# Kernel optimization log

Measured on AMD Instinct MI355X. Metric: run time of the kernel, lower is better.

Reference implementation:

```python
import jax, jax.numpy as jnp
import numpy as np

N = 100000   # nodes
E = 1600000  # edges
D = 128      # input feat
H = 128      # hidden
C = 2        # out classes
EPS = 1e-5


def setup_inputs() -> dict:
    key = jax.random.key(0)
    ks = jax.random.split(key, 12)
    s = 0.05
    return {
        "x": jax.random.normal(ks[0], (N, D), jnp.float32),
        "W1": jax.random.normal(ks[1], (D, H), jnp.float32) * s,
        "b1": jnp.zeros((H,), jnp.float32),
        "g1": jnp.ones((H,), jnp.float32),
        "be1": jnp.zeros((H,), jnp.float32),
        "W2": jax.random.normal(ks[2], (H, H), jnp.float32) * s,
        "b2": jnp.zeros((H,), jnp.float32),
        "g2": jnp.ones((H,), jnp.float32),
        "be2": jnp.zeros((H,), jnp.float32),
        "W3": jax.random.normal(ks[3], (H, C), jnp.float32) * s,
        "b3": jnp.zeros((C,), jnp.float32),
        "edge_index": jax.random.randint(ks[4], (2, E), 0, N, dtype=jnp.int32),
    }


def _gcn_conv(x, W, b, src, dst, dis, di):
    h = x @ W                                   # [N, H]
    coef = (dis[src] * dis[dst])[:, None]       # per-edge norm
    msg = h[src] * coef                         # [E, H] gather
    agg = jax.ops.segment_sum(msg, dst, num_segments=x.shape[0])  # scatter-add
    agg = agg + h * di[:, None]                 # self-loop term (1/deg_i)
    return agg + b


def _bn(x, g, be):
    mu = x.mean(0)
    var = x.var(0)
    return (x - mu) * jax.lax.rsqrt(var + EPS) * g + be


def reference(x, W1, b1, g1, be1, W2, b2, g2, be2, W3, b3, edge_index):
    src, dst = edge_index[0], edge_index[1]
    n = x.shape[0]
    deg = jax.ops.segment_sum(jnp.ones((src.shape[0],), x.dtype), dst, num_segments=n) + 1.0
    dis = jax.lax.rsqrt(deg)
    di = 1.0 / deg
    h = jax.nn.relu(_bn(_gcn_conv(x, W1, b1, src, dst, dis, di), g1, be1))
    h = jax.nn.relu(_bn(_gcn_conv(h, W2, b2, src, dst, dis, di), g2, be2))
    h = _gcn_conv(h, W3, b3, src, dst, dis, di)
    return jax.nn.softmax(h, axis=1)
```

## Files before the change

kernel.cpp:

```cpp
#include <hip/hip_runtime.h>

#define NN 100000
#define NE 1600000
#define DF 128
#define NH (NN * DF)
#define EPS 1e-5f
#define NB 196
#define CAP 10240
#define EPB 8192
#define STB 512

typedef unsigned int uint;
typedef unsigned short ushort;
typedef __attribute__((ext_vector_type(8))) short bf16x8;
typedef __attribute__((ext_vector_type(4))) float f32x4;

__device__ __forceinline__ ushort f2bf(float f) {
    uint u = __float_as_uint(f);
    u += 0x7fffu + ((u >> 16) & 1u);
    return (ushort)(u >> 16);
}
__device__ __forceinline__ float bflo(uint u) { return __uint_as_float(u << 16); }
__device__ __forceinline__ float bfhi(uint u) { return __uint_as_float(u & 0xffff0000u); }

__launch_bounds__(256)
__global__ void k_part(const int* __restrict__ src, const int* __restrict__ dst,
                       int* __restrict__ gcur, uint* __restrict__ ebuf) {
    __shared__ int cnt[NB], base[NB];
    int t = threadIdx.x;
    if (t < NB) cnt[t] = 0;
    __syncthreads();
    int e0 = blockIdx.x * EPB;
#pragma unroll
    for (int i = 0; i < EPB / 256; ++i) {
        int e = e0 + i * 256 + t;
        if (e < NE) atomicAdd(&cnt[dst[e] >> 9], 1);
    }
    __syncthreads();
    if (t < NB) {
        base[t] = atomicAdd(&gcur[t], cnt[t]);
        cnt[t] = 0;
    }
    __syncthreads();
#pragma unroll
    for (int i = 0; i < EPB / 256; ++i) {
        int e = e0 + i * 256 + t;
        if (e < NE) {
            int d = dst[e];
            int b = d >> 9;
            int off = atomicAdd(&cnt[b], 1);
            ebuf[b * CAP + base[b] + off] = (uint)src[e] | ((uint)(d & 511) << 17);
        }
    }
}

__global__ void k_bscan(const int* __restrict__ gcur, int* __restrict__ bstart,
                        int* __restrict__ rp) {
    __shared__ int sh[256];
    int t = threadIdx.x;
    int v = (t < NB) ? gcur[t] : 0;
    sh[t] = v;
    __syncthreads();
    for (int off = 1; off < 256; off <<= 1) {
        int x = (t >= off) ? sh[t - off] : 0;
        __syncthreads();
        sh[t] += x;
        __syncthreads();
    }
    if (t < NB) bstart[t] = sh[t] - v;
    if (t == 0) {
        bstart[NB] = NE;
        rp[NN] = NE;
    }
}

__launch_bounds__(256)
__global__ void k_c1(const uint* __restrict__ ebuf, const int* __restrict__ gcur,
                     const int* __restrict__ bstart, float* __restrict__ dis,
                     float* __restrict__ di, int* __restrict__ rp) {
    __shared__ int ncnt[512];
    __shared__ int ssum[256];
    int b = blockIdx.x, t = threadIdx.x;
    ncnt[t] = 0;
    ncnt[t + 256] = 0;
    __syncthreads();
    int ne = gcur[b];
    const uint* eb = ebuf + (size_t)b * CAP;
    for (int e = t; e < ne; e += 256) atomicAdd(&ncnt[eb[e] >> 17], 1);
    __syncthreads();
    int a0 = ncnt[t * 2], a1 = ncnt[t * 2 + 1];
    int ps = a0 + a1;
    ssum[t] = ps;
    __syncthreads();
    for (int off = 1; off < 256; off <<= 1) {
        int x = (t >= off) ? ssum[t - off] : 0;
        __syncthreads();
        ssum[t] += x;
        __syncthreads();
    }
    int excl = ssum[t] - ps;
    int base = bstart[b];
    int g0 = b * 512 + t * 2;
    if (g0 < NN) {
        rp[g0] = base + excl;
        float d = (float)a0 + 1.0f;
        dis[g0] = rsqrtf(d);
        di[g0] = 1.0f / d;
    }
    if (g0 + 1 < NN) {
        rp[g0 + 1] = base + excl + a0;
        float d = (float)a1 + 1.0f;
        dis[g0 + 1] = rsqrtf(d);
        di[g0 + 1] = 1.0f / d;
    }
}

__launch_bounds__(256)
__global__ void k_c2(const uint* __restrict__ ebuf, const int* __restrict__ gcur,
                     const int* __restrict__ rp, const float* __restrict__ dis,
                     uint2* __restrict__ ec) {
    __shared__ int cur[512];
    __shared__ float dl[512];
    int b = blockIdx.x, t = threadIdx.x;
#pragma unroll
    for (int i = 0; i < 2; ++i) {
        int g = b * 512 + t + i * 256;
        if (g < NN) {
            cur[t + i * 256] = rp[g];
            dl[t + i * 256] = dis[g];
        }
    }
    __syncthreads();
    int ne = gcur[b];
    const uint* eb = ebuf + (size_t)b * CAP;
    for (int e = t; e < ne; e += 256) {
        uint u = eb[e];
        int s = u & 0x1FFFF;
        int dloc = u >> 17;
        int pos = atomicAdd(&cur[dloc], 1);
        ec[pos] = make_uint2((uint)s, __float_as_uint(dis[s] * dl[dloc]));
    }
}

__global__ void k_cvt_x(const float* __restrict__ X, ushort* __restrict__ Xb) {
    int t = blockIdx.x * blockDim.x + threadIdx.x;
    if (t >= NH / 8) return;
    const float4* X4 = (const float4*)X;
    float4 v0 = X4[t * 2], v1 = X4[t * 2 + 1];
    uint4 o;
    o.x = (uint)f2bf(v0.x) | ((uint)f2bf(v0.y) << 16);
    o.y = (uint)f2bf(v0.z) | ((uint)f2bf(v0.w) << 16);
    o.z = (uint)f2bf(v1.x) | ((uint)f2bf(v1.y) << 16);
    o.w = (uint)f2bf(v1.z) | ((uint)f2bf(v1.w) << 16);
    ((uint4*)Xb)[t] = o;
}

__global__ void k_cvt_w(const float* __restrict__ W, ushort* __restrict__ Wt) {
    int id = blockIdx.x * blockDim.x + threadIdx.x;
    int n = id & 127, k = id >> 7;
    ushort b = f2bf(W[id]);
    int byte = n * 256 + (((k >> 3) ^ (n & 7)) << 4) + ((k & 7) << 1);
    *(ushort*)((char*)Wt + byte) = b;
}

__launch_bounds__(256, 2)
__global__ void k_mm_mfma(const ushort* __restrict__ Xb, const ushort* __restrict__ Wt,
                          const float* __restrict__ par, ushort* __restrict__ Y,
                          int nrows) {
    __shared__ uint4 ws4[2048];
    char* ws = (char*)ws4;
    const int tid = threadIdx.x;
    const int wv = tid >> 6, l = tid & 63;
    const int l15 = l & 15, l4 = l >> 4;
    const int row_base = blockIdx.x * 128 + wv * 32;
    const bool act = row_base < nrows;

    bf16x8 a[2][4];
    if (act) {
#pragma unroll
        for (int mt = 0; mt < 2; ++mt)
#pragma unroll
            for (int ks = 0; ks < 4; ++ks) {
                int r = row_base + mt * 16 + l15;
                a[mt][ks] = *(const bf16x8*)&Xb[(size_t)r * 128 + ks * 32 + l4 * 8];
            }
        if (par) {
#pragma unroll
            for (int ks = 0; ks < 4; ++ks) {
                int k0 = ks * 32 + l4 * 8;
                float4 sa = *(const float4*)&par[k0];
                float4 sb = *(const float4*)&par[k0 + 4];
                float4 ha = *(const float4*)&par[128 + k0];
                float4 hb = *(const float4*)&par[128 + k0 + 4];
                float sc[8] = {sa.x, sa.y, sa.z, sa.w, sb.x, sb.y, sb.z, sb.w};
                float sh[8] = {ha.x, ha.y, ha.z, ha.w, hb.x, hb.y, hb.z, hb.w};
#pragma unroll
                for (int mt = 0; mt < 2; ++mt)
#pragma unroll
                    for (int j = 0; j < 8; ++j) {
                        float f = __uint_as_float(((uint)(ushort)a[mt][ks][j]) << 16);
                        f = fmaxf(f * sc[j] + sh[j], 0.0f);
                        a[mt][ks][j] = (short)f2bf(f);
                    }
            }
        }
    }
    const uint4* Wg = (const uint4*)Wt;
#pragma unroll
    for (int i = 0; i < 8; ++i) ws4[tid + i * 256] = Wg[tid + i * 256];
    __syncthreads();
    if (!act) return;

    f32x4 acc[2][8];
#pragma unroll
    for (int mt = 0; mt < 2; ++mt)
#pragma unroll
        for (int nt = 0; nt < 8; ++nt) acc[mt][nt] = (f32x4){0.f, 0.f, 0.f, 0.f};

#pragma unroll
    for (int ks = 0; ks < 4; ++ks) {
        bf16x8 b[8];
#pragma unroll
        for (int nt = 0; nt < 8; ++nt) {
            int n = nt * 16 + l15;
            int chunk = (ks * 4 + l4) ^ (n & 7);
            b[nt] = *(const bf16x8*)(ws + n * 256 + chunk * 16);
        }
#pragma unroll
        for (int nt = 0; nt < 8; ++nt) {
            acc[0][nt] = __builtin_amdgcn_mfma_f32_16x16x32_bf16(a[0][ks], b[nt], acc[0][nt], 0, 0, 0);
            acc[1][nt] = __builtin_amdgcn_mfma_f32_16x16x32_bf16(a[1][ks], b[nt], acc[1][nt], 0, 0, 0);
        }
    }
#pragma unroll
    for (int mt = 0; mt < 2; ++mt)
#pragma unroll
        for (int nt = 0; nt < 8; ++nt)
#pragma unroll
            for (int r = 0; r < 4; ++r) {
                int ro = row_base + mt * 16 + l4 * 4 + r;
                Y[(size_t)ro * 128 + nt * 16 + l15] = f2bf(acc[mt][nt][r]);
            }
}

__launch_bounds__(256)
__global__ void k_gather_b(const ushort* __restrict__ H, const int* __restrict__ rp,
                           const uint2* __restrict__ ec, const float* __restrict__ di,
                           const float* __restrict__ b, uint* __restrict__ outb) {
    int wid = (int)(((long long)blockIdx.x * blockDim.x + threadIdx.x) >> 6);
    int lane = threadIdx.x & 63;
    if (wid >= NN) return;
    int beg = rp[wid], end = rp[wid + 1];
    float dv = di[wid];
    const uint* H32 = (const uint*)H;
    uint hu = H32[(size_t)wid * 64 + lane];
    float2 bb = *(const float2*)&b[lane * 2];
    float ax = bflo(hu) * dv + bb.x;
    float ay = bfhi(hu) * dv + bb.y;
    int i = beg;
    for (; i + 3 < end; i += 4) {
        uint2 e0 = ec[i], e1 = ec[i + 1], e2 = ec[i + 2], e3 = ec[i + 3];
        uint u0 = H32[(size_t)e0.x * 64 + lane];
        uint u1 = H32[(size_t)e1.x * 64 + lane];
        uint u2 = H32[(size_t)e2.x * 64 + lane];
        uint u3 = H32[(size_t)e3.x * 64 + lane];
        float c0 = __uint_as_float(e0.y), c1 = __uint_as_float(e1.y);
        float c2 = __uint_as_float(e2.y), c3 = __uint_as_float(e3.y);
        ax += bflo(u0) * c0 + bflo(u1) * c1 + bflo(u2) * c2 + bflo(u3) * c3;
        ay += bfhi(u0) * c0 + bfhi(u1) * c1 + bfhi(u2) * c2 + bfhi(u3) * c3;
    }
    for (; i < end; ++i) {
        uint2 e0 = ec[i];
        uint u = H32[(size_t)e0.x * 64 + lane];
        float c = __uint_as_float(e0.y);
        ax += bflo(u) * c;
        ay += bfhi(u) * c;
    }
    outb[(size_t)wid * 64 + lane] = (uint)f2bf(ax) | ((uint)f2bf(ay) << 16);
}

__launch_bounds__(256)
__global__ void k_statsb(const uint* __restrict__ V, float* __restrict__ partial,
                         int nrows) {
    int cp = threadIdx.x & 63;
    int q = threadIdx.x >> 6;
    float s0 = 0.f, s1 = 0.f, q0 = 0.f, q1 = 0.f;
    for (int r = blockIdx.x * 4 + q; r < nrows; r += STB * 4) {
        uint u = V[(size_t)r * 64 + cp];
        float lo = bflo(u), hi = bfhi(u);
        s0 += lo;
        q0 += lo * lo;
        s1 += hi;
        q1 += hi * hi;
    }
    __shared__ float L[4][256];
    L[0][threadIdx.x] = s0;
    L[1][threadIdx.x] = s1;
    L[2][threadIdx.x] = q0;
    L[3][threadIdx.x] = q1;
    __syncthreads();
    if (q == 0) {
        float a = 0.f, b = 0.f, c = 0.f, d = 0.f;
#pragma unroll
        for (int j = 0; j < 4; ++j) {
            a += L[0][cp + j * 64];
            b += L[1][cp + j * 64];
            c += L[2][cp + j * 64];
            d += L[3][cp + j * 64];
        }
        float* P = partial + (size_t)blockIdx.x * 256;
        P[2 * cp] = a;
        P[2 * cp + 1] = b;
        P[128 + 2 * cp] = c;
        P[128 + 2 * cp + 1] = d;
    }
}

__global__ void k_red(const float* __restrict__ partial, const float* __restrict__ g,
                      const float* __restrict__ be, float* __restrict__ par) {
    int c = threadIdx.x;
    float acc = 0.f;
    for (int b = 0; b < STB; ++b) acc += partial[b * 256 + c];
    __shared__ float sh[256];
    sh[c] = acc;
    __syncthreads();
    if (c < 128) {
        float mu = sh[c] * (1.0f / NN);
        float var = sh[c + 128] * (1.0f / NN) - mu * mu;
        float inv = rsqrtf(var + EPS);
        float scv = inv * g[c];
        par[c] = scv;
        par[128 + c] = be[c] - mu * scv;
    }
}

__global__ void k_mm2(const uint* __restrict__ X, const float* __restrict__ W3,
                      const float* __restrict__ par, float* __restrict__ Z) {
    int wid = (int)(((long long)blockIdx.x * blockDim.x + threadIdx.x) >> 6);
    int lane = threadIdx.x & 63;
    if (wid >= NN) return;
    uint xu = X[(size_t)wid * 64 + lane];
    float2 sc = *(const float2*)&par[2 * lane];
    float2 sh = *(const float2*)&par[128 + 2 * lane];
    float x0 = fmaxf(bflo(xu) * sc.x + sh.x, 0.f);
    float x1 = fmaxf(bfhi(xu) * sc.y + sh.y, 0.f);
    float4 w4 = *(const float4*)&W3[lane * 4];
    float p0 = x0 * w4.x + x1 * w4.z;
    float p1 = x0 * w4.y + x1 * w4.w;
#pragma unroll
    for (int off = 32; off; off >>= 1) {
        p0 += __shfl_xor(p0, off);
        p1 += __shfl_xor(p1, off);
    }
    if (lane == 0) *(float2*)&Z[wid * 2] = make_float2(p0, p1);
}

__global__ void k_l3(const float* __restrict__ Z, const int* __restrict__ rp,
                     const uint2* __restrict__ ec, const float* __restrict__ di,
                     const float* __restrict__ b3, float* __restrict__ out) {
    int n = blockIdx.x * blockDim.x + threadIdx.x;
    if (n >= NN) return;
    int beg = rp[n], end = rp[n + 1];
    float dv = di[n];
    float2 z = *(const float2*)&Z[n * 2];
    float a0 = z.x * dv + b3[0];
    float a1 = z.y * dv + b3[1];
    for (int i = beg; i < end; ++i) {
        uint2 e0 = ec[i];
        float c = __uint_as_float(e0.y);
        float2 v = *(const float2*)&Z[e0.x * 2];
        a0 += v.x * c;
        a1 += v.y * c;
    }
    float m = fmaxf(a0, a1);
    float e0 = __expf(a0 - m), e1 = __expf(a1 - m);
    float inv = 1.0f / (e0 + e1);
    *(float2*)&out[n * 2] = make_float2(e0 * inv, e1 * inv);
}

extern "C" void kernel_launch(void* const* d_in, const int* in_sizes, int n_in,
                              void* d_out, int out_size, void* d_ws, size_t ws_size,
                              hipStream_t stream) {
    const float* x  = (const float*)d_in[0];
    const float* W1 = (const float*)d_in[1];
    const float* b1 = (const float*)d_in[2];
    const float* g1 = (const float*)d_in[3];
    const float* be1= (const float*)d_in[4];
    const float* W2 = (const float*)d_in[5];
    const float* b2 = (const float*)d_in[6];
    const float* g2 = (const float*)d_in[7];
    const float* be2= (const float*)d_in[8];
    const float* W3 = (const float*)d_in[9];
    const float* b3 = (const float*)d_in[10];
    const int*   ei = (const int*)d_in[11];
    const int* srcp = ei;
    const int* dstp = ei + NE;
    float* out = (float*)d_out;

    char* wsp = (char*)d_ws;
    auto alloc = [&](size_t bytes) {
        char* p = wsp;
        wsp += (bytes + 255) & ~(size_t)255;
        return p;
    };
    ushort* Xb   = (ushort*)alloc((size_t)NH * 2);
    ushort* Hb   = (ushort*)alloc((size_t)NH * 2);
    uint*   AGGb = (uint*)alloc((size_t)NN * 64 * 4);
    ushort* Wt   = (ushort*)alloc(16384 * 2);
    float*  Z    = (float*)alloc((size_t)2 * NN * 4);
    float*  dis  = (float*)alloc((size_t)NN * 4);
    float*  di   = (float*)alloc((size_t)NN * 4);
    float*  partial = (float*)alloc((size_t)STB * 256 * 4);
    float*  par  = (float*)alloc(512 * 4);
    uint2*  ec   = (uint2*)alloc((size_t)NE * 8);
    uint*   ebuf = (uint*)alloc((size_t)NB * CAP * 4);
    int*    gcur = (int*)alloc(NB * 4);
    int*    bstart=(int*)alloc((NB + 1) * 4);
    int*    rp   = (int*)alloc((size_t)(NN + 1) * 4);
    float*  par1 = par;
    float*  par2 = par + 256;

    const int B = 256;
    const int gN  = (NN + B - 1) / B;
    const int gMM = (NN + 127) / 128;
    const int gW  = (int)(((long long)NN * 64 + B - 1) / B);
    const int gCV = (NH / 8 + B - 1) / B;
    const int gPT = (NE + EPB - 1) / EPB;

    hipMemsetAsync(gcur, 0, NB * sizeof(int), stream);
    k_part<<<gPT, B, 0, stream>>>(srcp, dstp, gcur, ebuf);
    k_bscan<<<1, 256, 0, stream>>>(gcur, bstart, rp);
    k_c1<<<NB, B, 0, stream>>>(ebuf, gcur, bstart, dis, di, rp);
    k_c2<<<NB, B, 0, stream>>>(ebuf, gcur, rp, dis, ec);
    k_cvt_x<<<gCV, B, 0, stream>>>(x, Xb);

    k_cvt_w<<<64, 256, 0, stream>>>(W1, Wt);
    k_mm_mfma<<<gMM, B, 0, stream>>>(Xb, Wt, nullptr, Hb, NN);
    k_gather_b<<<gW, B, 0, stream>>>(Hb, rp, ec, di, b1, AGGb);
    k_statsb<<<STB, B, 0, stream>>>(AGGb, partial, NN);
    k_red<<<1, 256, 0, stream>>>(partial, g1, be1, par1);

    k_cvt_w<<<64, 256, 0, stream>>>(W2, Wt);
    k_mm_mfma<<<gMM, B, 0, stream>>>((const ushort*)AGGb, Wt, par1, Hb, NN);
    k_gather_b<<<gW, B, 0, stream>>>(Hb, rp, ec, di, b2, AGGb);
    k_statsb<<<STB, B, 0, stream>>>(AGGb, partial, NN);
    k_red<<<1, 256, 0, stream>>>(partial, g2, be2, par2);

    k_mm2<<<gW, B, 0, stream>>>(AGGb, W3, par2, Z);
    k_l3<<<gN, B, 0, stream>>>(Z, rp, ec, di, b3, out);
}
```

Measured before the change: 448.9 us.

## Fuse BN stats into gather, fold x conversion into GEMM, drop scan kernel

Three kernels are folded into their neighbours. The batch-norm statistics are now accumulated inside a persistent grid-stride gather kernel, which removes a separate pass that re-read the aggregated features. The fp32-to-bf16 conversion of x moves into the first MFMA GEMM through a template mode, and the bucket prefix scan is recomputed per block inside k_c1. The gather inner loop is also unrolled to 8 edges for more memory-level parallelism. In exchange, the statistics now use fp32 values rather than the bf16-rounded ones, the GEMM reads twice as many bytes for x, and fewer gather blocks run.

```diff
diff --git a/kernel.cpp b/kernel.cpp
--- a/kernel.cpp
+++ b/kernel.cpp
@@ -8,7 +8,7 @@
 #define NB 196
 #define CAP 10240
 #define EPB 8192
-#define STB 512
+#define GB 1024
 
 typedef unsigned int uint;
 typedef unsigned short ushort;
@@ -54,36 +54,27 @@
     }
 }
 
-__global__ void k_bscan(const int* __restrict__ gcur, int* __restrict__ bstart,
-                        int* __restrict__ rp) {
-    __shared__ int sh[256];
-    int t = threadIdx.x;
-    int v = (t < NB) ? gcur[t] : 0;
-    sh[t] = v;
-    __syncthreads();
-    for (int off = 1; off < 256; off <<= 1) {
-        int x = (t >= off) ? sh[t - off] : 0;
-        __syncthreads();
-        sh[t] += x;
-        __syncthreads();
-    }
-    if (t < NB) bstart[t] = sh[t] - v;
-    if (t == 0) {
-        bstart[NB] = NE;
-        rp[NN] = NE;
-    }
-}
-
 __launch_bounds__(256)
 __global__ void k_c1(const uint* __restrict__ ebuf, const int* __restrict__ gcur,
-                     const int* __restrict__ bstart, float* __restrict__ dis,
-                     float* __restrict__ di, int* __restrict__ rp) {
+                     float* __restrict__ dis, float* __restrict__ di,
+                     int* __restrict__ rp) {
     __shared__ int ncnt[512];
     __shared__ int ssum[256];
+    __shared__ int bsh[256];
+    __shared__ int sbase;
     int b = blockIdx.x, t = threadIdx.x;
+    bsh[t] = (t < b && t < NB) ? gcur[t] : 0;
     ncnt[t] = 0;
     ncnt[t + 256] = 0;
     __syncthreads();
+    for (int off = 128; off; off >>= 1) {
+        if (t < off) bsh[t] += bsh[t + off];
+        __syncthreads();
+    }
+    if (t == 0) sbase = bsh[0];
+    __syncthreads();
+    int base = sbase;
+
     int ne = gcur[b];
     const uint* eb = ebuf + (size_t)b * CAP;
     for (int e = t; e < ne; e += 256) atomicAdd(&ncnt[eb[e] >> 17], 1);
@@ -99,7 +90,6 @@
         __syncthreads();
     }
     int excl = ssum[t] - ps;
-    int base = bstart[b];
     int g0 = b * 512 + t * 2;
     if (g0 < NN) {
         rp[g0] = base + excl;
@@ -113,6 +103,7 @@
         dis[g0 + 1] = rsqrtf(d);
         di[g0 + 1] = 1.0f / d;
     }
+    if (b == NB - 1 && t == 0) rp[NN] = NE;
 }
 
 __launch_bounds__(256)
@@ -142,19 +133,6 @@
     }
 }
 
-__global__ void k_cvt_x(const float* __restrict__ X, ushort* __restrict__ Xb) {
-    int t = blockIdx.x * blockDim.x + threadIdx.x;
-    if (t >= NH / 8) return;
-    const float4* X4 = (const float4*)X;
-    float4 v0 = X4[t * 2], v1 = X4[t * 2 + 1];
-    uint4 o;
-    o.x = (uint)f2bf(v0.x) | ((uint)f2bf(v0.y) << 16);
-    o.y = (uint)f2bf(v0.z) | ((uint)f2bf(v0.w) << 16);
-    o.z = (uint)f2bf(v1.x) | ((uint)f2bf(v1.y) << 16);
-    o.w = (uint)f2bf(v1.z) | ((uint)f2bf(v1.w) << 16);
-    ((uint4*)Xb)[t] = o;
-}
-
 __global__ void k_cvt_w(const float* __restrict__ W, ushort* __restrict__ Wt) {
     int id = blockIdx.x * blockDim.x + threadIdx.x;
     int n = id & 127, k = id >> 7;
@@ -163,8 +141,9 @@
     *(ushort*)((char*)Wt + byte) = b;
 }
 
+template <int MODE>
 __launch_bounds__(256, 2)
-__global__ void k_mm_mfma(const ushort* __restrict__ Xb, const ushort* __restrict__ Wt,
+__global__ void k_mm_mfma(const void* __restrict__ Xv, const ushort* __restrict__ Wt,
                           const float* __restrict__ par, ushort* __restrict__ Y,
                           int nrows) {
     __shared__ uint4 ws4[2048];
@@ -182,9 +161,22 @@
 #pragma unroll
             for (int ks = 0; ks < 4; ++ks) {
                 int r = row_base + mt * 16 + l15;
-                a[mt][ks] = *(const bf16x8*)&Xb[(size_t)r * 128 + ks * 32 + l4 * 8];
+                if (MODE == 2) {
+                    const float* Xf = (const float*)Xv;
+                    float4 f0 = *(const float4*)&Xf[(size_t)r * 128 + ks * 32 + l4 * 8];
+                    float4 f1 = *(const float4*)&Xf[(size_t)r * 128 + ks * 32 + l4 * 8 + 4];
+                    bf16x8 v;
+                    v[0] = (short)f2bf(f0.x); v[1] = (short)f2bf(f0.y);
+                    v[2] = (short)f2bf(f0.z); v[3] = (short)f2bf(f0.w);
+                    v[4] = (short)f2bf(f1.x); v[5] = (short)f2bf(f1.y);
+                    v[6] = (short)f2bf(f1.z); v[7] = (short)f2bf(f1.w);
+                    a[mt][ks] = v;
+                } else {
+                    const ushort* Xb = (const ushort*)Xv;
+                    a[mt][ks] = *(const bf16x8*)&Xb[(size_t)r * 128 + ks * 32 + l4 * 8];
+                }
             }
-        if (par) {
+        if (MODE == 1) {
 #pragma unroll
             for (int ks = 0; ks < 4; ++ks) {
                 int k0 = ks * 32 + l4 * 8;
@@ -246,73 +238,72 @@
 __launch_bounds__(256)
 __global__ void k_gather_b(const ushort* __restrict__ H, const int* __restrict__ rp,
                            const uint2* __restrict__ ec, const float* __restrict__ di,
-                           const float* __restrict__ b, uint* __restrict__ outb) {
-    int wid = (int)(((long long)blockIdx.x * blockDim.x + threadIdx.x) >> 6);
-    int lane = threadIdx.x & 63;
-    if (wid >= NN) return;
-    int beg = rp[wid], end = rp[wid + 1];
-    float dv = di[wid];
+                           const float* __restrict__ b, uint* __restrict__ outb,
+                           float* __restrict__ partial) {
+    int wv = threadIdx.x >> 6, lane = threadIdx.x & 63;
     const uint* H32 = (const uint*)H;
-    uint hu = H32[(size_t)wid * 64 + lane];
     float2 bb = *(const float2*)&b[lane * 2];
-    float ax = bflo(hu) * dv + bb.x;
-    float ay = bfhi(hu) * dv + bb.y;
-    int i = beg;
-    for (; i + 3 < end; i += 4) {
-        uint2 e0 = ec[i], e1 = ec[i + 1], e2 = ec[i + 2], e3 = ec[i + 3];
-        uint u0 = H32[(size_t)e0.x * 64 + lane];
-        uint u1 = H32[(size_t)e1.x * 64 + lane];
-        uint u2 = H32[(size_t)e2.x * 64 + lane];
-        uint u3 = H32[(size_t)e3.x * 64 + lane];
-        float c0 = __uint_as_float(e0.y), c1 = __uint_as_float(e1.y);
-        float c2 = __uint_as_float(e2.y), c3 = __uint_as_float(e3.y);
-        ax += bflo(u0) * c0 + bflo(u1) * c1 + bflo(u2) * c2 + bflo(u3) * c3;
-        ay += bfhi(u0) * c0 + bfhi(u1) * c1 + bfhi(u2) * c2 + bfhi(u3) * c3;
-    }
-    for (; i < end; ++i) {
-        uint2 e0 = ec[i];
-        uint u = H32[(size_t)e0.x * 64 + lane];
-        float c = __uint_as_float(e0.y);
-        ax += bflo(u) * c;
-        ay += bfhi(u) * c;
-    }
-    outb[(size_t)wid * 64 + lane] = (uint)f2bf(ax) | ((uint)f2bf(ay) << 16);
-}
-
-__launch_bounds__(256)
-__global__ void k_statsb(const uint* __restrict__ V, float* __restrict__ partial,
-                         int nrows) {
-    int cp = threadIdx.x & 63;
-    int q = threadIdx.x >> 6;
     float s0 = 0.f, s1 = 0.f, q0 = 0.f, q1 = 0.f;
-    for (int r = blockIdx.x * 4 + q; r < nrows; r += STB * 4) {
-        uint u = V[(size_t)r * 64 + cp];
-        float lo = bflo(u), hi = bfhi(u);
-        s0 += lo;
-        q0 += lo * lo;
-        s1 += hi;
-        q1 += hi * hi;
-    }
-    __shared__ float L[4][256];
-    L[0][threadIdx.x] = s0;
-    L[1][threadIdx.x] = s1;
-    L[2][threadIdx.x] = q0;
-    L[3][threadIdx.x] = q1;
-    __syncthreads();
-    if (q == 0) {
-        float a = 0.f, b = 0.f, c = 0.f, d = 0.f;
-#pragma unroll
-        for (int j = 0; j < 4; ++j) {
-            a += L[0][cp + j * 64];
-            b += L[1][cp + j * 64];
-            c += L[2][cp + j * 64];
-            d += L[3][cp + j * 64];
-        }
-        float* P = partial + (size_t)blockIdx.x * 256;
-        P[2 * cp] = a;
-        P[2 * cp + 1] = b;
-        P[128 + 2 * cp] = c;
-        P[128 + 2 * cp + 1] = d;
+
+    for (int wid = blockIdx.x * 4 + wv; wid < NN; wid += GB * 4) {
+        int beg = rp[wid], end = rp[wid + 1];
+        float dv = di[wid];
+        uint hu = H32[(size_t)wid * 64 + lane];
+        float ax = bflo(hu) * dv + bb.x;
+        float ay = bfhi(hu) * dv + bb.y;
+        int i = beg;
+        for (; i + 7 < end; i += 8) {
+            uint2 e[8];
+            uint u[8];
+#pragma unroll
+            for (int j = 0; j < 8; ++j) e[j] = ec[i + j];
+#pragma unroll
+            for (int j = 0; j < 8; ++j) u[j] = H32[(size_t)e[j].x * 64 + lane];
+#pragma unroll
+            for (int j = 0; j < 8; ++j) {
+                float c = __uint_as_float(e[j].y);
+                ax += bflo(u[j]) * c;
+                ay += bfhi(u[j]) * c;
+            }
+        }
+        for (; i + 3 < end; i += 4) {
+            uint2 e[4];
+            uint u[4];
+#pragma unroll
+            for (int j = 0; j < 4; ++j) e[j] = ec[i + j];
+#pragma unroll
+            for (int j = 0; j < 4; ++j) u[j] = H32[(size_t)e[j].x * 64 + lane];
+#pragma unroll
+            for (int j = 0; j < 4; ++j) {
+                float c = __uint_as_float(e[j].y);
+                ax += bflo(u[j]) * c;
+                ay += bfhi(u[j]) * c;
+            }
+        }
+        for (; i < end; ++i) {
+            uint2 e0 = ec[i];
+            uint u = H32[(size_t)e0.x * 64 + lane];
+            float c = __uint_as_float(e0.y);
+            ax += bflo(u) * c;
+            ay += bfhi(u) * c;
+        }
+        outb[(size_t)wid * 64 + lane] = (uint)f2bf(ax) | ((uint)f2bf(ay) << 16);
+        s0 += ax; q0 += ax * ax;
+        s1 += ay; q1 += ay * ay;
+    }
+
+    __shared__ float Ls[4][128], Lq[4][128];
+    Ls[wv][2 * lane] = s0;
+    Ls[wv][2 * lane + 1] = s1;
+    Lq[wv][2 * lane] = q0;
+    Lq[wv][2 * lane + 1] = q1;
+    __syncthreads();
+    int t = threadIdx.x;
+    if (t < 128)
+        partial[(size_t)blockIdx.x * 256 + t] = Ls[0][t] + Ls[1][t] + Ls[2][t] + Ls[3][t];
+    else {
+        int c = t - 128;
+        partial[(size_t)blockIdx.x * 256 + t] = Lq[0][c] + Lq[1][c] + Lq[2][c] + Lq[3][c];
     }
 }
 
@@ -320,7 +311,7 @@
                       const float* __restrict__ be, float* __restrict__ par) {
     int c = threadIdx.x;
     float acc = 0.f;
-    for (int b = 0; b < STB; ++b) acc += partial[b * 256 + c];
+    for (int b = 0; b < GB; ++b) acc += partial[b * 256 + c];
     __shared__ float sh[256];
     sh[c] = acc;
     __syncthreads();
@@ -403,19 +394,17 @@
         wsp += (bytes + 255) & ~(size_t)255;
         return p;
     };
-    ushort* Xb   = (ushort*)alloc((size_t)NH * 2);
     ushort* Hb   = (ushort*)alloc((size_t)NH * 2);
     uint*   AGGb = (uint*)alloc((size_t)NN * 64 * 4);
     ushort* Wt   = (ushort*)alloc(16384 * 2);
     float*  Z    = (float*)alloc((size_t)2 * NN * 4);
     float*  dis  = (float*)alloc((size_t)NN * 4);
     float*  di   = (float*)alloc((size_t)NN * 4);
-    float*  partial = (float*)alloc((size_t)STB * 256 * 4);
+    float*  partial = (float*)alloc((size_t)GB * 256 * 4);
     float*  par  = (float*)alloc(512 * 4);
     uint2*  ec   = (uint2*)alloc((size_t)NE * 8);
     uint*   ebuf = (uint*)alloc((size_t)NB * CAP * 4);
     int*    gcur = (int*)alloc(NB * 4);
-    int*    bstart=(int*)alloc((NB + 1) * 4);
     int*    rp   = (int*)alloc((size_t)(NN + 1) * 4);
     float*  par1 = par;
     float*  par2 = par + 256;
@@ -424,26 +413,21 @@
     const int gN  = (NN + B - 1) / B;
     const int gMM = (NN + 127) / 128;
     const int gW  = (int)(((long long)NN * 64 + B - 1) / B);
-    const int gCV = (NH / 8 + B - 1) / B;
     const int gPT = (NE + EPB - 1) / EPB;
 
     hipMemsetAsync(gcur, 0, NB * sizeof(int), stream);
     k_part<<<gPT, B, 0, stream>>>(srcp, dstp, gcur, ebuf);
-    k_bscan<<<1, 256, 0, stream>>>(gcur, bstart, rp);
-    k_c1<<<NB, B, 0, stream>>>(ebuf, gcur, bstart, dis, di, rp);
+    k_c1<<<NB, B, 0, stream>>>(ebuf, gcur, dis, di, rp);
     k_c2<<<NB, B, 0, stream>>>(ebuf, gcur, rp, dis, ec);
-    k_cvt_x<<<gCV, B, 0, stream>>>(x, Xb);
 
     k_cvt_w<<<64, 256, 0, stream>>>(W1, Wt);
-    k_mm_mfma<<<gMM, B, 0, stream>>>(Xb, Wt, nullptr, Hb, NN);
-    k_gather_b<<<gW, B, 0, stream>>>(Hb, rp, ec, di, b1, AGGb);
-    k_statsb<<<STB, B, 0, stream>>>(AGGb, partial, NN);
+    k_mm_mfma<2><<<gMM, B, 0, stream>>>(x, Wt, nullptr, Hb, NN);
+    k_gather_b<<<GB, B, 0, stream>>>(Hb, rp, ec, di, b1, AGGb, partial);
     k_red<<<1, 256, 0, stream>>>(partial, g1, be1, par1);
 
     k_cvt_w<<<64, 256, 0, stream>>>(W2, Wt);
-    k_mm_mfma<<<gMM, B, 0, stream>>>((const ushort*)AGGb, Wt, par1, Hb, NN);
-    k_gather_b<<<gW, B, 0, stream>>>(Hb, rp, ec, di, b2, AGGb);
-    k_statsb<<<STB, B, 0, stream>>>(AGGb, partial, NN);
+    k_mm_mfma<1><<<gMM, B, 0, stream>>>(AGGb, Wt, par1, Hb, NN);
+    k_gather_b<<<GB, B, 0, stream>>>(Hb, rp, ec, di, b2, AGGb, partial);
     k_red<<<1, 256, 0, stream>>>(partial, g2, be2, par2);
 
     k_mm2<<<gW, B, 0, stream>>>(AGGb, W3, par2, Z);
```

Measured after the change: 456.6 us. About the same (+1.7%).
